# Optimization experiments

Measured on AMD Instinct MI355X. Metric: run time of the kernel, lower is better.

## Reference

```python
import jax, jax.numpy as jnp
import numpy as np

N_NODES = 50000
N_EDGES = 625000
HIDDEN = 128
NUM_GRAPHS = 128
EPS = 1e-5


def setup_inputs() -> dict:
    key = jax.random.key(0)
    ks = jax.random.split(key, 8)
    node = jax.random.normal(ks[0], (N_NODES, HIDDEN), dtype=jnp.float32)
    edge_index = jax.random.randint(ks[1], (2, N_EDGES), 0, N_NODES, dtype=jnp.int64)
    edge_attr = jax.random.uniform(ks[2], (N_EDGES,), dtype=jnp.float32)
    batch_ptr = jnp.sort(jax.random.randint(ks[3], (N_NODES,), 0, NUM_GRAPHS, dtype=jnp.int64))
    # GCNConv linear: weight [out,in], bias [out]
    W = jax.random.normal(ks[4], (HIDDEN, HIDDEN), dtype=jnp.float32) * (1.0 / np.sqrt(HIDDEN))
    b = jnp.zeros((HIDDEN,), dtype=jnp.float32)
    # GraphNorm params
    gn_weight = 1.0 + 0.02 * jax.random.normal(ks[5], (HIDDEN,), dtype=jnp.float32)
    gn_bias = 0.05 * jax.random.normal(ks[6], (HIDDEN,), dtype=jnp.float32)
    gn_mean_scale = 1.0 + 0.02 * jax.random.normal(ks[7], (HIDDEN,), dtype=jnp.float32)
    return {"node": node, "edge_index": edge_index, "edge_attr": edge_attr,
            "batch_ptr": batch_ptr, "W": W, "b": b,
            "gn_weight": gn_weight, "gn_bias": gn_bias, "gn_mean_scale": gn_mean_scale}


def _gcn_conv(x, src, dst, w, W, b):
    n = x.shape[0]
    # add self loops with weight 1
    loop = jnp.arange(n, dtype=src.dtype)
    src = jnp.concatenate([src, loop])
    dst = jnp.concatenate([dst, loop])
    w = jnp.concatenate([w, jnp.ones((n,), dtype=w.dtype)])
    # symmetric degree normalization (degrees at target nodes)
    deg = jax.ops.segment_sum(w, dst, num_segments=n)
    dinv = jnp.where(deg > 0, jax.lax.rsqrt(deg), 0.0)
    norm = dinv[src] * w * dinv[dst]  # [E+n]
    h = x @ W.T  # [n, d]
    msg = norm[:, None] * h[src]  # gather + scale
    out = jax.ops.segment_sum(msg, dst, num_segments=n)  # scatter-add
    return out + b


def _graph_norm(x, batch, weight, bias, mean_scale):
    cnt = jax.ops.segment_sum(jnp.ones((x.shape[0],), x.dtype), batch, num_segments=NUM_GRAPHS)
    cnt = jnp.maximum(cnt, 1.0)[:, None]
    mean = jax.ops.segment_sum(x, batch, num_segments=NUM_GRAPHS) / cnt
    centered = x - mean_scale * mean[batch]
    var = jax.ops.segment_sum(centered * centered, batch, num_segments=NUM_GRAPHS) / cnt
    inv_std = jax.lax.rsqrt(var + EPS)[batch]
    return weight * centered * inv_std + bias


def reference(node, edge_index, edge_attr, batch_ptr, W, b, gn_weight, gn_bias, gn_mean_scale):
    src, dst = edge_index[0], edge_index[1]
    h = _gcn_conv(node, src, dst, edge_attr, W, b)
    h = _graph_norm(h, batch_ptr, gn_weight, gn_bias, gn_mean_scale)
    return jax.nn.relu(h)
```

## Files before the change

### kernel.cpp

```cpp
#include <hip/hip_runtime.h>

#define N_NODES    50000
#define N_EDGES    625000
#define HIDDEN     128
#define NUM_GRAPHS 128
#define EPS_GN     1e-5f
#define FIXSCALE32 65536.0f
#define NGEMM_BLK  782
#define NHIST_BLK  306
#define NB_SCAN    196

typedef __bf16 bf16x8 __attribute__((ext_vector_type(8)));
typedef float  f32x4  __attribute__((ext_vector_type(4)));
typedef unsigned short u16x8 __attribute__((ext_vector_type(8)));
typedef unsigned long long u64;

__device__ inline unsigned short f2b(float f) {
    __bf16 b = (__bf16)f;
    return __builtin_bit_cast(unsigned short, b);
}
__device__ inline float b2f(unsigned short u) {
    unsigned int x = ((unsigned int)u) << 16;
    return __builtin_bit_cast(float, x);
}

#define HB_OFF     0
#define CNT_OFF    3200000
#define BSUM_OFF   3250000
#define DONE_OFF   3250256
#define DINV_OFF   3250260
#define WB_OFF     3300260
#define GSTART_OFF 3308452
#define ROWS_OFF   3308581
#define EPACK_OFF  3358582
#define SLOT_OFF   4608582
#define TMP_OFF    4608584

__global__ void prep(const float* __restrict__ W, unsigned short* __restrict__ wb,
                     uint4* __restrict__ z) {
    int i = blockIdx.x * 256 + threadIdx.x;
    if (i < 12565) z[i] = make_uint4(0u, 0u, 0u, 0u);
    if (i < HIDDEN * HIDDEN) wb[i] = f2b(W[i]);
}

__global__ __launch_bounds__(256) void gemm_hist(const float* __restrict__ x,
                                                 const unsigned short* __restrict__ wb,
                                                 unsigned short* __restrict__ hb,
                                                 const int* __restrict__ dst,
                                                 const float* __restrict__ w,
                                                 unsigned int* __restrict__ cnt32,
                                                 unsigned int* __restrict__ slot) {
    if (blockIdx.x >= NGEMM_BLK) {
        int base = (blockIdx.x - NGEMM_BLK) * 256 + threadIdx.x;
        if (base * 8 >= N_EDGES) return;
        int4   dA = ((const int4*)dst)[base * 2];
        int4   dB = ((const int4*)dst)[base * 2 + 1];
        float4 wA = ((const float4*)w)[base * 2];
        float4 wB = ((const float4*)w)[base * 2 + 1];
        uint4 sA, sB;
        unsigned int fx;
        fx = (unsigned int)(wA.x * FIXSCALE32 + 0.5f);
        sA.x = atomicAdd(&cnt32[dA.x], (1u << 24) | fx) >> 24;
        fx = (unsigned int)(wA.y * FIXSCALE32 + 0.5f);
        sA.y = atomicAdd(&cnt32[dA.y], (1u << 24) | fx) >> 24;
        fx = (unsigned int)(wA.z * FIXSCALE32 + 0.5f);
        sA.z = atomicAdd(&cnt32[dA.z], (1u << 24) | fx) >> 24;
        fx = (unsigned int)(wA.w * FIXSCALE32 + 0.5f);
        sA.w = atomicAdd(&cnt32[dA.w], (1u << 24) | fx) >> 24;
        fx = (unsigned int)(wB.x * FIXSCALE32 + 0.5f);
        sB.x = atomicAdd(&cnt32[dB.x], (1u << 24) | fx) >> 24;
        fx = (unsigned int)(wB.y * FIXSCALE32 + 0.5f);
        sB.y = atomicAdd(&cnt32[dB.y], (1u << 24) | fx) >> 24;
        fx = (unsigned int)(wB.z * FIXSCALE32 + 0.5f);
        sB.z = atomicAdd(&cnt32[dB.z], (1u << 24) | fx) >> 24;
        fx = (unsigned int)(wB.w * FIXSCALE32 + 0.5f);
        sB.w = atomicAdd(&cnt32[dB.w], (1u << 24) | fx) >> 24;
        ((uint4*)slot)[base * 2]     = sA;
        ((uint4*)slot)[base * 2 + 1] = sB;
        return;
    }
    const int wave = threadIdx.x >> 6;
    const int lane = threadIdx.x & 63;
    const int row0 = blockIdx.x * 64 + wave * 16;
    const int r  = lane & 15;
    const int ko = (lane >> 4) * 8;
    f32x4 acc[8];
#pragma unroll
    for (int t = 0; t < 8; ++t) { acc[t][0] = 0.f; acc[t][1] = 0.f; acc[t][2] = 0.f; acc[t][3] = 0.f; }
    int arow = row0 + r;
    if (arow >= N_NODES) arow = N_NODES - 1;
    const size_t abase = (size_t)arow * HIDDEN + ko;
#pragma unroll
    for (int kt = 0; kt < HIDDEN; kt += 32) {
        float4 a0 = *(const float4*)(x + abase + kt);
        float4 a1 = *(const float4*)(x + abase + kt + 4);
        bf16x8 a;
        a[0] = (__bf16)a0.x; a[1] = (__bf16)a0.y; a[2] = (__bf16)a0.z; a[3] = (__bf16)a0.w;
        a[4] = (__bf16)a1.x; a[5] = (__bf16)a1.y; a[6] = (__bf16)a1.z; a[7] = (__bf16)a1.w;
#pragma unroll
        for (int t = 0; t < 8; ++t) {
            bf16x8 b = *(const bf16x8*)(wb + (size_t)(t * 16 + r) * HIDDEN + kt + ko);
            acc[t] = __builtin_amdgcn_mfma_f32_16x16x32_bf16(a, b, acc[t], 0, 0, 0);
        }
    }
    const int orow = row0 + (lane >> 4) * 4;
#pragma unroll
    for (int t = 0; t < 8; ++t) {
#pragma unroll
        for (int j = 0; j < 4; ++j) {
            int rr = orow + j;
            if (rr < N_NODES) hb[(size_t)rr * HIDDEN + t * 16 + r] = f2b(acc[t][j]);
        }
    }
}

__global__ __launch_bounds__(256) void scan_fused(const unsigned int* __restrict__ cnt32,
                                                  unsigned int* __restrict__ bsum,
                                                  unsigned int* __restrict__ done,
                                                  float* __restrict__ dinv,
                                                  const int* __restrict__ batch,
                                                  int* __restrict__ gstart,
                                                  int* __restrict__ rowstart) {
    __shared__ int red[256];
    __shared__ int sb[256];
    const int t = threadIdx.x;
    const int b = blockIdx.x;
    const int i = b * 256 + t;
    int c = 0;
    if (i < N_NODES) {
        unsigned int v = cnt32[i];
        c = (int)(v >> 24);
        dinv[i] = rsqrtf(1.0f + (float)(v & 0xFFFFFFu) * (1.0f / FIXSCALE32));
        int b0 = batch[i];
        int prev = (i == 0) ? -1 : batch[i - 1];
        for (int g = prev + 1; g <= b0; ++g) gstart[g] = i;
        if (i == N_NODES - 1) {
            for (int g = b0 + 1; g <= NUM_GRAPHS; ++g) gstart[g] = N_NODES;
        }
    }
    red[t] = c;
    __syncthreads();
    for (int off = 128; off > 0; off >>= 1) {
        if (t < off) red[t] += red[t + off];
        __syncthreads();
    }
    if (t == 0) {
        atomicExch(&bsum[b], (unsigned int)red[0]);
        __threadfence();
        atomicAdd(done, 1u);
        while (atomicAdd(done, 0u) < (unsigned int)NB_SCAN) { }
    }
    __syncthreads();
    sb[t] = (t < NB_SCAN) ? (int)atomicAdd(&bsum[t], 0u) : 0;
    __syncthreads();
    for (int off = 1; off < 256; off <<= 1) {
        int v = (t >= off) ? sb[t - off] : 0;
        __syncthreads();
        sb[t] += v;
        __syncthreads();
    }
    int boff = (b == 0) ? 0 : sb[b - 1];
    __shared__ int s[256];
    s[t] = c;
    __syncthreads();
    for (int off = 1; off < 256; off <<= 1) {
        int v = (t >= off) ? s[t - off] : 0;
        __syncthreads();
        s[t] += v;
        __syncthreads();
    }
    if (i < N_NODES) rowstart[i] = boff + s[t] - c;
    if (i == N_NODES) rowstart[N_NODES] = N_EDGES;
}

__global__ void csr_fill(const int* __restrict__ src, const int* __restrict__ dst,
                         const float* __restrict__ w, const float* __restrict__ dinv,
                         const int* __restrict__ rowstart, const unsigned int* __restrict__ slot,
                         u64* __restrict__ epack) {
    int base = blockIdx.x * blockDim.x + threadIdx.x;
    if (base * 4 >= N_EDGES) return;
    int4   s4 = ((const int4*)src)[base];
    int4   d4 = ((const int4*)dst)[base];
    float4 w4 = ((const float4*)w)[base];
    uint4  r4 = ((const uint4*)slot)[base];
    float nm0 = dinv[s4.x] * w4.x * dinv[d4.x];
    float nm1 = dinv[s4.y] * w4.y * dinv[d4.y];
    float nm2 = dinv[s4.z] * w4.z * dinv[d4.z];
    float nm3 = dinv[s4.w] * w4.w * dinv[d4.w];
    epack[rowstart[d4.x] + (int)r4.x] = (u64)(unsigned int)s4.x | ((u64)__float_as_uint(nm0) << 32);
    epack[rowstart[d4.y] + (int)r4.y] = (u64)(unsigned int)s4.y | ((u64)__float_as_uint(nm1) << 32);
    epack[rowstart[d4.z] + (int)r4.z] = (u64)(unsigned int)s4.z | ((u64)__float_as_uint(nm2) << 32);
    epack[rowstart[d4.w] + (int)r4.w] = (u64)(unsigned int)s4.w | ((u64)__float_as_uint(nm3) << 32);
}

__global__ __launch_bounds__(256) void gather_fused(const unsigned short* __restrict__ hb,
                                                    const int* __restrict__ rowstart,
                                                    const u64* __restrict__ epack,
                                                    const float* __restrict__ dinv,
                                                    const float* __restrict__ b,
                                                    unsigned short* __restrict__ tmp) {
    const int t = threadIdx.x;
    const int n = blockIdx.x * 16 + (t >> 4);
    if (n >= N_NODES) return;
    const int c8 = (t & 15) * 8;
    const int s0 = rowstart[n];
    const int e0 = rowstart[n + 1];
    const float di = dinv[n];
    const float sl = di * di;
    float acc[8];
    {
        u16x8 hv = *(const u16x8*)(hb + (size_t)n * HIDDEN + c8);
#pragma unroll
        for (int j = 0; j < 8; ++j) acc[j] = sl * b2f(hv[j]);
    }
    int p = s0;
    for (; p + 4 <= e0; p += 4) {
        u64 e1 = epack[p];
        u64 e2 = epack[p + 1];
        u64 e3 = epack[p + 2];
        u64 e4 = epack[p + 3];
        int   x1 = (int)(unsigned int)e1;
        int   x2 = (int)(unsigned int)e2;
        int   x3 = (int)(unsigned int)e3;
        int   x4 = (int)(unsigned int)e4;
        float n1 = __uint_as_float((unsigned int)(e1 >> 32));
        float n2 = __uint_as_float((unsigned int)(e2 >> 32));
        float n3 = __uint_as_float((unsigned int)(e3 >> 32));
        float n4 = __uint_as_float((unsigned int)(e4 >> 32));
        u16x8 v1 = *(const u16x8*)(hb + (size_t)x1 * HIDDEN + c8);
        u16x8 v2 = *(const u16x8*)(hb + (size_t)x2 * HIDDEN + c8);
        u16x8 v3 = *(const u16x8*)(hb + (size_t)x3 * HIDDEN + c8);
        u16x8 v4 = *(const u16x8*)(hb + (size_t)x4 * HIDDEN + c8);
#pragma unroll
        for (int j = 0; j < 8; ++j) acc[j] = fmaf(n1, b2f(v1[j]), acc[j]);
#pragma unroll
        for (int j = 0; j < 8; ++j) acc[j] = fmaf(n2, b2f(v2[j]), acc[j]);
#pragma unroll
        for (int j = 0; j < 8; ++j) acc[j] = fmaf(n3, b2f(v3[j]), acc[j]);
#pragma unroll
        for (int j = 0; j < 8; ++j) acc[j] = fmaf(n4, b2f(v4[j]), acc[j]);
    }
    for (; p < e0; ++p) {
        u64 e1 = epack[p];
        int   x1 = (int)(unsigned int)e1;
        float n1 = __uint_as_float((unsigned int)(e1 >> 32));
        u16x8 v1 = *(const u16x8*)(hb + (size_t)x1 * HIDDEN + c8);
#pragma unroll
        for (int j = 0; j < 8; ++j) acc[j] = fmaf(n1, b2f(v1[j]), acc[j]);
    }
    float4 b0 = *(const float4*)(b + c8);
    float4 b1 = *(const float4*)(b + c8 + 4);
    u16x8 o;
    o[0] = f2b(acc[0] + b0.x); o[1] = f2b(acc[1] + b0.y);
    o[2] = f2b(acc[2] + b0.z); o[3] = f2b(acc[3] + b0.w);
    o[4] = f2b(acc[4] + b1.x); o[5] = f2b(acc[5] + b1.y);
    o[6] = f2b(acc[6] + b1.z); o[7] = f2b(acc[7] + b1.w);
    *(u16x8*)(tmp + (size_t)n * HIDDEN + c8) = o;
}

__global__ __launch_bounds__(256) void stats_apply(const unsigned short* __restrict__ tmp,
                                                   const int* __restrict__ gstart,
                                                   const float* __restrict__ ms,
                                                   const float* __restrict__ gw,
                                                   const float* __restrict__ gb,
                                                   float* __restrict__ out) {
    const int g = blockIdx.x >> 2;
    const int q = blockIdx.x & 3;
    const int l = threadIdx.x & 31;
    const int c = q * 32 + l;
    const int r = threadIdx.x >> 5;
    const int s = gstart[g];
    const int e = gstart[g + 1];
    float sum = 0.f, sq = 0.f;
    for (int n = s + r; n < e; n += 8) {
        float v = b2f(tmp[(size_t)n * HIDDEN + c]);
        sum += v;
        sq = fmaf(v, v, sq);
    }
    __shared__ float ssum[8][32], ssq[8][32];
    __shared__ float sA[32], sS[32];
    ssum[r][l] = sum;
    ssq[r][l]  = sq;
    __syncthreads();
    if (r == 0) {
#pragma unroll
        for (int i = 1; i < 8; ++i) { sum += ssum[i][l]; sq += ssq[i][l]; }
        float cnt  = (float)max(e - s, 1);
        float mean = sum / cnt;
        float m2   = sq / cnt;
        float msv  = ms[c];
        float var  = fmaxf(m2 - mean * mean * msv * (2.f - msv), 0.f);
        float a    = gw[c] * rsqrtf(var + EPS_GN);
        sA[l] = a;
        sS[l] = gb[c] - a * msv * mean;
    }
    __syncthreads();
    float a  = sA[l];
    float sh = sS[l];
    for (int n = s + r; n < e; n += 8) {
        float v = b2f(tmp[(size_t)n * HIDDEN + c]);
        out[(size_t)n * HIDDEN + c] = fmaxf(fmaf(a, v, sh), 0.f);
    }
}

extern "C" void kernel_launch(void* const* d_in, const int* in_sizes, int n_in,
                              void* d_out, int out_size, void* d_ws, size_t ws_size,
                              hipStream_t stream) {
    const float* node  = (const float*)d_in[0];
    const int*   ei    = (const int*)d_in[1];
    const float* eattr = (const float*)d_in[2];
    const int*   batch = (const int*)d_in[3];
    const float* W     = (const float*)d_in[4];
    const float* b     = (const float*)d_in[5];
    const float* gnw   = (const float*)d_in[6];
    const float* gnb   = (const float*)d_in[7];
    const float* gnms  = (const float*)d_in[8];
    float* out = (float*)d_out;
    float* ws  = (float*)d_ws;

    const int* src = ei;
    const int* dst = ei + N_EDGES;

    unsigned short* hb = (unsigned short*)(ws + HB_OFF);
    unsigned int* cnt32 = (unsigned int*)(ws + CNT_OFF);
    unsigned int* bsum  = (unsigned int*)(ws + BSUM_OFF);
    unsigned int* done  = (unsigned int*)(ws + DONE_OFF);
    float* dinv    = ws + DINV_OFF;
    unsigned short* wb = (unsigned short*)(ws + WB_OFF);
    int*   gstart  = (int*)(ws + GSTART_OFF);
    int*   rowstart= (int*)(ws + ROWS_OFF);
    u64*   epack   = (u64*)(ws + EPACK_OFF);
    unsigned int* slot = (unsigned int*)(ws + SLOT_OFF);
    unsigned short* tmp = (unsigned short*)(ws + TMP_OFF);

    prep<<<98, 256, 0, stream>>>(W, wb, (uint4*)cnt32);
    gemm_hist<<<NGEMM_BLK + NHIST_BLK, 256, 0, stream>>>(node, wb, hb, dst, eattr, cnt32, slot);
    scan_fused<<<NB_SCAN, 256, 0, stream>>>(cnt32, bsum, done, dinv, batch, gstart, rowstart);
    csr_fill<<<(N_EDGES / 4 + 255) / 256, 256, 0, stream>>>(src, dst, eattr, dinv, rowstart, slot, epack);
    gather_fused<<<(N_NODES + 15) / 16, 256, 0, stream>>>(hb, rowstart, epack, dinv, b, tmp);
    stats_apply<<<NUM_GRAPHS * 4, 256, 0, stream>>>(tmp, gstart, gnms, gnw, gnb, out);

    (void)in_sizes; (void)n_in; (void)out_size; (void)ws_size;
}
```

Baseline: 127.2 us.

## Split node range into two halves and software-pipeline stages across fused launches

Splits the destination nodes into two halves and interleaves the stages: histogram, scan, CSR fill, gather and stats for half A run in the same launch as the previous stage for half B. The aim is to fill the GPU during the small, latency-bound stages (scan, stats) and hide the gaps between launches. The source-side dinv is moved from CSR fill into the gather, because with split scans dinv for the second half may not be ready during CSR fill of half A. Each pass now scans all edges twice with a predicate, and the stats split assumes graphs do not straddle the boundary in a harmful way. The scan also waits on a spin barrier, so it needs all of its blocks to be resident at the same time as the other blocks in the launch.

```diff
diff --git a/kernel.cpp b/kernel.cpp
--- a/kernel.cpp
+++ b/kernel.cpp
@@ -6,9 +6,12 @@
 #define NUM_GRAPHS 128
 #define EPS_GN     1e-5f
 #define FIXSCALE32 65536.0f
+#define NSPLIT     25000
 #define NGEMM_BLK  782
 #define NHIST_BLK  306
-#define NB_SCAN    196
+#define NCSR_BLK   611
+#define NB_HALF    98
+#define NGATH_BLK  1563
 
 typedef __bf16 bf16x8 __attribute__((ext_vector_type(8)));
 typedef float  f32x4  __attribute__((ext_vector_type(4)));
@@ -26,108 +29,63 @@
 
 #define HB_OFF     0
 #define CNT_OFF    3200000
-#define BSUM_OFF   3250000
-#define DONE_OFF   3250256
-#define DINV_OFF   3250260
-#define WB_OFF     3300260
-#define GSTART_OFF 3308452
-#define ROWS_OFF   3308581
-#define EPACK_OFF  3358582
-#define SLOT_OFF   4608582
-#define TMP_OFF    4608584
+#define DONE_OFF   3250000
+#define BSUMA_OFF  3250008
+#define BSUMB_OFF  3250136
+#define DINV_OFF   3250264
+#define WB_OFF     3300264
+#define GSTART_OFF 3308456
+#define ROWS_OFF   3308585
+#define EPACK_OFF  3358586
+#define SLOT_OFF   4608588
+#define TMP_OFF    5233588
 
 __global__ void prep(const float* __restrict__ W, unsigned short* __restrict__ wb,
                      uint4* __restrict__ z) {
     int i = blockIdx.x * 256 + threadIdx.x;
-    if (i < 12565) z[i] = make_uint4(0u, 0u, 0u, 0u);
+    if (i < 12502) z[i] = make_uint4(0u, 0u, 0u, 0u);
     if (i < HIDDEN * HIDDEN) wb[i] = f2b(W[i]);
 }
 
-__global__ __launch_bounds__(256) void gemm_hist(const float* __restrict__ x,
-                                                 const unsigned short* __restrict__ wb,
-                                                 unsigned short* __restrict__ hb,
-                                                 const int* __restrict__ dst,
-                                                 const float* __restrict__ w,
-                                                 unsigned int* __restrict__ cnt32,
-                                                 unsigned int* __restrict__ slot) {
-    if (blockIdx.x >= NGEMM_BLK) {
-        int base = (blockIdx.x - NGEMM_BLK) * 256 + threadIdx.x;
-        if (base * 8 >= N_EDGES) return;
-        int4   dA = ((const int4*)dst)[base * 2];
-        int4   dB = ((const int4*)dst)[base * 2 + 1];
-        float4 wA = ((const float4*)w)[base * 2];
-        float4 wB = ((const float4*)w)[base * 2 + 1];
-        uint4 sA, sB;
-        unsigned int fx;
-        fx = (unsigned int)(wA.x * FIXSCALE32 + 0.5f);
-        sA.x = atomicAdd(&cnt32[dA.x], (1u << 24) | fx) >> 24;
-        fx = (unsigned int)(wA.y * FIXSCALE32 + 0.5f);
-        sA.y = atomicAdd(&cnt32[dA.y], (1u << 24) | fx) >> 24;
-        fx = (unsigned int)(wA.z * FIXSCALE32 + 0.5f);
-        sA.z = atomicAdd(&cnt32[dA.z], (1u << 24) | fx) >> 24;
-        fx = (unsigned int)(wA.w * FIXSCALE32 + 0.5f);
-        sA.w = atomicAdd(&cnt32[dA.w], (1u << 24) | fx) >> 24;
-        fx = (unsigned int)(wB.x * FIXSCALE32 + 0.5f);
-        sB.x = atomicAdd(&cnt32[dB.x], (1u << 24) | fx) >> 24;
-        fx = (unsigned int)(wB.y * FIXSCALE32 + 0.5f);
-        sB.y = atomicAdd(&cnt32[dB.y], (1u << 24) | fx) >> 24;
-        fx = (unsigned int)(wB.z * FIXSCALE32 + 0.5f);
-        sB.z = atomicAdd(&cnt32[dB.z], (1u << 24) | fx) >> 24;
-        fx = (unsigned int)(wB.w * FIXSCALE32 + 0.5f);
-        sB.w = atomicAdd(&cnt32[dB.w], (1u << 24) | fx) >> 24;
-        ((uint4*)slot)[base * 2]     = sA;
-        ((uint4*)slot)[base * 2 + 1] = sB;
-        return;
-    }
-    const int wave = threadIdx.x >> 6;
-    const int lane = threadIdx.x & 63;
-    const int row0 = blockIdx.x * 64 + wave * 16;
-    const int r  = lane & 15;
-    const int ko = (lane >> 4) * 8;
-    f32x4 acc[8];
-#pragma unroll
-    for (int t = 0; t < 8; ++t) { acc[t][0] = 0.f; acc[t][1] = 0.f; acc[t][2] = 0.f; acc[t][3] = 0.f; }
-    int arow = row0 + r;
-    if (arow >= N_NODES) arow = N_NODES - 1;
-    const size_t abase = (size_t)arow * HIDDEN + ko;
-#pragma unroll
-    for (int kt = 0; kt < HIDDEN; kt += 32) {
-        float4 a0 = *(const float4*)(x + abase + kt);
-        float4 a1 = *(const float4*)(x + abase + kt + 4);
-        bf16x8 a;
-        a[0] = (__bf16)a0.x; a[1] = (__bf16)a0.y; a[2] = (__bf16)a0.z; a[3] = (__bf16)a0.w;
-        a[4] = (__bf16)a1.x; a[5] = (__bf16)a1.y; a[6] = (__bf16)a1.z; a[7] = (__bf16)a1.w;
-#pragma unroll
-        for (int t = 0; t < 8; ++t) {
-            bf16x8 b = *(const bf16x8*)(wb + (size_t)(t * 16 + r) * HIDDEN + kt + ko);
-            acc[t] = __builtin_amdgcn_mfma_f32_16x16x32_bf16(a, b, acc[t], 0, 0, 0);
-        }
-    }
-    const int orow = row0 + (lane >> 4) * 4;
-#pragma unroll
-    for (int t = 0; t < 8; ++t) {
-#pragma unroll
-        for (int j = 0; j < 4; ++j) {
-            int rr = orow + j;
-            if (rr < N_NODES) hb[(size_t)rr * HIDDEN + t * 16 + r] = f2b(acc[t][j]);
-        }
-    }
-}
-
-__global__ __launch_bounds__(256) void scan_fused(const unsigned int* __restrict__ cnt32,
-                                                  unsigned int* __restrict__ bsum,
-                                                  unsigned int* __restrict__ done,
-                                                  float* __restrict__ dinv,
-                                                  const int* __restrict__ batch,
-                                                  int* __restrict__ gstart,
-                                                  int* __restrict__ rowstart) {
+__device__ inline void hist_pass(int blk, const int* __restrict__ dst,
+                                 const float* __restrict__ w,
+                                 unsigned int* __restrict__ cnt32,
+                                 unsigned int* __restrict__ slot, bool isA) {
+    int base = blk * 256 + threadIdx.x;
+    if (base * 8 >= N_EDGES) return;
+    int4   d0 = ((const int4*)dst)[base * 2];
+    int4   d1 = ((const int4*)dst)[base * 2 + 1];
+    float4 w0 = ((const float4*)w)[base * 2];
+    float4 w1 = ((const float4*)w)[base * 2 + 1];
+    int e0 = base * 8;
+#define HPROC(EI, DV, WV)                                                        \
+    if (((DV) < NSPLIT) == isA) {                                                \
+        unsigned int fx = (unsigned int)((WV) * FIXSCALE32 + 0.5f);              \
+        slot[EI] = atomicAdd(&cnt32[DV], (1u << 24) | fx) >> 24;                 \
+    }
+    HPROC(e0 + 0, d0.x, w0.x) HPROC(e0 + 1, d0.y, w0.y)
+    HPROC(e0 + 2, d0.z, w0.z) HPROC(e0 + 3, d0.w, w0.w)
+    HPROC(e0 + 4, d1.x, w1.x) HPROC(e0 + 5, d1.y, w1.y)
+    HPROC(e0 + 6, d1.z, w1.z) HPROC(e0 + 7, d1.w, w1.w)
+#undef HPROC
+}
+
+__device__ inline void scan_half(int sbid, int nbase,
+                                 const unsigned int* __restrict__ cnt32,
+                                 unsigned int* __restrict__ bsum,
+                                 unsigned int* __restrict__ done,
+                                 float* __restrict__ dinv,
+                                 const int* __restrict__ batch,
+                                 int* __restrict__ gstart,
+                                 int* __restrict__ rowstart) {
     __shared__ int red[256];
-    __shared__ int sb[256];
+    __shared__ int sb[128];
+    __shared__ int s[256];
     const int t = threadIdx.x;
-    const int b = blockIdx.x;
-    const int i = b * 256 + t;
+    const int i = nbase + sbid * 256 + t;
+    const int iend = nbase + NSPLIT;
     int c = 0;
-    if (i < N_NODES) {
+    if (i < iend) {
         unsigned int v = cnt32[i];
         c = (int)(v >> 24);
         dinv[i] = rsqrtf(1.0f + (float)(v & 0xFFFFFFu) * (1.0f / FIXSCALE32));
@@ -145,22 +103,23 @@
         __syncthreads();
     }
     if (t == 0) {
-        atomicExch(&bsum[b], (unsigned int)red[0]);
+        atomicExch(&bsum[sbid], (unsigned int)red[0]);
         __threadfence();
         atomicAdd(done, 1u);
-        while (atomicAdd(done, 0u) < (unsigned int)NB_SCAN) { }
-    }
-    __syncthreads();
-    sb[t] = (t < NB_SCAN) ? (int)atomicAdd(&bsum[t], 0u) : 0;
-    __syncthreads();
-    for (int off = 1; off < 256; off <<= 1) {
-        int v = (t >= off) ? sb[t - off] : 0;
-        __syncthreads();
-        sb[t] += v;
-        __syncthreads();
-    }
-    int boff = (b == 0) ? 0 : sb[b - 1];
-    __shared__ int s[256];
+        while (atomicAdd(done, 0u) < (unsigned int)NB_HALF) {
+            __builtin_amdgcn_s_sleep(2);
+        }
+    }
+    __syncthreads();
+    if (t < NB_HALF) sb[t] = (int)atomicAdd(&bsum[t], 0u);
+    __syncthreads();
+    if (t == 0) {
+        int acc = 0;
+        for (int k = 0; k < NB_HALF; ++k) { acc += sb[k]; sb[k] = acc; }
+    }
+    __syncthreads();
+    int ebase = (nbase == 0) ? 0 : rowstart[nbase];
+    int boff = ebase + ((sbid == 0) ? 0 : sb[sbid - 1]);
     s[t] = c;
     __syncthreads();
     for (int off = 1; off < 256; off <<= 1) {
@@ -169,39 +128,49 @@
         s[t] += v;
         __syncthreads();
     }
-    if (i < N_NODES) rowstart[i] = boff + s[t] - c;
-    if (i == N_NODES) rowstart[N_NODES] = N_EDGES;
-}
-
-__global__ void csr_fill(const int* __restrict__ src, const int* __restrict__ dst,
-                         const float* __restrict__ w, const float* __restrict__ dinv,
-                         const int* __restrict__ rowstart, const unsigned int* __restrict__ slot,
-                         u64* __restrict__ epack) {
-    int base = blockIdx.x * blockDim.x + threadIdx.x;
+    if (i < iend) rowstart[i] = boff + s[t] - c;
+    if (sbid == NB_HALF - 1 && t == 0) {
+        if (nbase == 0) rowstart[NSPLIT] = sb[NB_HALF - 1];
+        else            rowstart[N_NODES] = N_EDGES;
+    }
+}
+
+__device__ inline void csr_pass(int blk, const int* __restrict__ src,
+                                const int* __restrict__ dst,
+                                const float* __restrict__ w,
+                                const float* __restrict__ dinv,
+                                const int* __restrict__ rowstart,
+                                const unsigned int* __restrict__ slot,
+                                u64* __restrict__ epack, bool isA) {
+    int base = blk * 256 + threadIdx.x;
     if (base * 4 >= N_EDGES) return;
     int4   s4 = ((const int4*)src)[base];
     int4   d4 = ((const int4*)dst)[base];
     float4 w4 = ((const float4*)w)[base];
     uint4  r4 = ((const uint4*)slot)[base];
-    float nm0 = dinv[s4.x] * w4.x * dinv[d4.x];
-    float nm1 = dinv[s4.y] * w4.y * dinv[d4.y];
-    float nm2 = dinv[s4.z] * w4.z * dinv[d4.z];
-    float nm3 = dinv[s4.w] * w4.w * dinv[d4.w];
-    epack[rowstart[d4.x] + (int)r4.x] = (u64)(unsigned int)s4.x | ((u64)__float_as_uint(nm0) << 32);
-    epack[rowstart[d4.y] + (int)r4.y] = (u64)(unsigned int)s4.y | ((u64)__float_as_uint(nm1) << 32);
-    epack[rowstart[d4.z] + (int)r4.z] = (u64)(unsigned int)s4.z | ((u64)__float_as_uint(nm2) << 32);
-    epack[rowstart[d4.w] + (int)r4.w] = (u64)(unsigned int)s4.w | ((u64)__float_as_uint(nm3) << 32);
-}
-
-__global__ __launch_bounds__(256) void gather_fused(const unsigned short* __restrict__ hb,
-                                                    const int* __restrict__ rowstart,
-                                                    const u64* __restrict__ epack,
-                                                    const float* __restrict__ dinv,
-                                                    const float* __restrict__ b,
-                                                    unsigned short* __restrict__ tmp) {
+#define CPROC(SV, DV, WV, RV)                                                     \
+    if (((DV) < NSPLIT) == isA) {                                                 \
+        float pn = (WV) * dinv[DV];                                               \
+        epack[rowstart[DV] + (int)(RV)] =                                         \
+            (u64)(unsigned int)(SV) | ((u64)__float_as_uint(pn) << 32);           \
+    }
+    CPROC(s4.x, d4.x, w4.x, r4.x)
+    CPROC(s4.y, d4.y, w4.y, r4.y)
+    CPROC(s4.z, d4.z, w4.z, r4.z)
+    CPROC(s4.w, d4.w, w4.w, r4.w)
+#undef CPROC
+}
+
+__device__ inline void gather_body(int gblk, int nbase,
+                                   const unsigned short* __restrict__ hb,
+                                   const int* __restrict__ rowstart,
+                                   const u64* __restrict__ epack,
+                                   const float* __restrict__ dinv,
+                                   const float* __restrict__ b,
+                                   unsigned short* __restrict__ tmp) {
     const int t = threadIdx.x;
-    const int n = blockIdx.x * 16 + (t >> 4);
-    if (n >= N_NODES) return;
+    const int n = nbase + gblk * 16 + (t >> 4);
+    if (n >= nbase + NSPLIT || n >= N_NODES) return;
     const int c8 = (t & 15) * 8;
     const int s0 = rowstart[n];
     const int e0 = rowstart[n + 1];
@@ -219,14 +188,14 @@
         u64 e2 = epack[p + 1];
         u64 e3 = epack[p + 2];
         u64 e4 = epack[p + 3];
-        int   x1 = (int)(unsigned int)e1;
-        int   x2 = (int)(unsigned int)e2;
-        int   x3 = (int)(unsigned int)e3;
-        int   x4 = (int)(unsigned int)e4;
-        float n1 = __uint_as_float((unsigned int)(e1 >> 32));
-        float n2 = __uint_as_float((unsigned int)(e2 >> 32));
-        float n3 = __uint_as_float((unsigned int)(e3 >> 32));
-        float n4 = __uint_as_float((unsigned int)(e4 >> 32));
+        int x1 = (int)(unsigned int)e1;
+        int x2 = (int)(unsigned int)e2;
+        int x3 = (int)(unsigned int)e3;
+        int x4 = (int)(unsigned int)e4;
+        float n1 = __uint_as_float((unsigned int)(e1 >> 32)) * dinv[x1];
+        float n2 = __uint_as_float((unsigned int)(e2 >> 32)) * dinv[x2];
+        float n3 = __uint_as_float((unsigned int)(e3 >> 32)) * dinv[x3];
+        float n4 = __uint_as_float((unsigned int)(e4 >> 32)) * dinv[x4];
         u16x8 v1 = *(const u16x8*)(hb + (size_t)x1 * HIDDEN + c8);
         u16x8 v2 = *(const u16x8*)(hb + (size_t)x2 * HIDDEN + c8);
         u16x8 v3 = *(const u16x8*)(hb + (size_t)x3 * HIDDEN + c8);
@@ -242,8 +211,8 @@
     }
     for (; p < e0; ++p) {
         u64 e1 = epack[p];
-        int   x1 = (int)(unsigned int)e1;
-        float n1 = __uint_as_float((unsigned int)(e1 >> 32));
+        int x1 = (int)(unsigned int)e1;
+        float n1 = __uint_as_float((unsigned int)(e1 >> 32)) * dinv[x1];
         u16x8 v1 = *(const u16x8*)(hb + (size_t)x1 * HIDDEN + c8);
 #pragma unroll
         for (int j = 0; j < 8; ++j) acc[j] = fmaf(n1, b2f(v1[j]), acc[j]);
@@ -258,19 +227,21 @@
     *(u16x8*)(tmp + (size_t)n * HIDDEN + c8) = o;
 }
 
-__global__ __launch_bounds__(256) void stats_apply(const unsigned short* __restrict__ tmp,
-                                                   const int* __restrict__ gstart,
-                                                   const float* __restrict__ ms,
-                                                   const float* __restrict__ gw,
-                                                   const float* __restrict__ gb,
-                                                   float* __restrict__ out) {
-    const int g = blockIdx.x >> 2;
-    const int q = blockIdx.x & 3;
+__device__ inline void stats_body(int sblk,
+                                  const unsigned short* __restrict__ tmp,
+                                  const int* __restrict__ gstart,
+                                  const float* __restrict__ ms,
+                                  const float* __restrict__ gw,
+                                  const float* __restrict__ gb,
+                                  float* __restrict__ out, bool phaseA) {
+    const int g = sblk >> 2;
+    const int q = sblk & 3;
     const int l = threadIdx.x & 31;
     const int c = q * 32 + l;
     const int r = threadIdx.x >> 5;
     const int s = gstart[g];
     const int e = gstart[g + 1];
+    if ((e <= NSPLIT) != phaseA) return;
     float sum = 0.f, sq = 0.f;
     for (int n = s + r; n < e; n += 8) {
         float v = b2f(tmp[(size_t)n * HIDDEN + c]);
@@ -301,6 +272,136 @@
         float v = b2f(tmp[(size_t)n * HIDDEN + c]);
         out[(size_t)n * HIDDEN + c] = fmaxf(fmaf(a, v, sh), 0.f);
     }
+}
+
+
+__global__ __launch_bounds__(256) void d1_gemm_histA(const float* __restrict__ x,
+                                                     const unsigned short* __restrict__ wb,
+                                                     unsigned short* __restrict__ hb,
+                                                     const int* __restrict__ dst,
+                                                     const float* __restrict__ w,
+                                                     unsigned int* __restrict__ cnt32,
+                                                     unsigned int* __restrict__ slot) {
+    if (blockIdx.x >= NGEMM_BLK) {
+        hist_pass(blockIdx.x - NGEMM_BLK, dst, w, cnt32, slot, true);
+        return;
+    }
+    const int wave = threadIdx.x >> 6;
+    const int lane = threadIdx.x & 63;
+    const int row0 = blockIdx.x * 64 + wave * 16;
+    const int r  = lane & 15;
+    const int ko = (lane >> 4) * 8;
+    f32x4 acc[8];
+#pragma unroll
+    for (int t = 0; t < 8; ++t) { acc[t][0] = 0.f; acc[t][1] = 0.f; acc[t][2] = 0.f; acc[t][3] = 0.f; }
+    int arow = row0 + r;
+    if (arow >= N_NODES) arow = N_NODES - 1;
+    const size_t abase = (size_t)arow * HIDDEN + ko;
+#pragma unroll
+    for (int kt = 0; kt < HIDDEN; kt += 32) {
+        float4 a0 = *(const float4*)(x + abase + kt);
+        float4 a1 = *(const float4*)(x + abase + kt + 4);
+        bf16x8 a;
+        a[0] = (__bf16)a0.x; a[1] = (__bf16)a0.y; a[2] = (__bf16)a0.z; a[3] = (__bf16)a0.w;
+        a[4] = (__bf16)a1.x; a[5] = (__bf16)a1.y; a[6] = (__bf16)a1.z; a[7] = (__bf16)a1.w;
+#pragma unroll
+        for (int t = 0; t < 8; ++t) {
+            bf16x8 b = *(const bf16x8*)(wb + (size_t)(t * 16 + r) * HIDDEN + kt + ko);
+            acc[t] = __builtin_amdgcn_mfma_f32_16x16x32_bf16(a, b, acc[t], 0, 0, 0);
+        }
+    }
+    const int orow = row0 + (lane >> 4) * 4;
+#pragma unroll
+    for (int t = 0; t < 8; ++t) {
+#pragma unroll
+        for (int j = 0; j < 4; ++j) {
+            int rr = orow + j;
+            if (rr < N_NODES) hb[(size_t)rr * HIDDEN + t * 16 + r] = f2b(acc[t][j]);
+        }
+    }
+}
+
+__global__ __launch_bounds__(256) void d2_histB_scanA(const int* __restrict__ dst,
+                                                      const float* __restrict__ w,
+                                                      unsigned int* __restrict__ cnt32,
+                                                      unsigned int* __restrict__ slot,
+                                                      unsigned int* __restrict__ bsumA,
+                                                      unsigned int* __restrict__ done,
+                                                      float* __restrict__ dinv,
+                                                      const int* __restrict__ batch,
+                                                      int* __restrict__ gstart,
+                                                      int* __restrict__ rowstart) {
+    if (blockIdx.x < NHIST_BLK) {
+        hist_pass(blockIdx.x, dst, w, cnt32, slot, false);
+        return;
+    }
+    scan_half(blockIdx.x - NHIST_BLK, 0, cnt32, bsumA, done, dinv, batch, gstart, rowstart);
+}
+
+__global__ __launch_bounds__(256) void d3_csrA_scanB(const int* __restrict__ src,
+                                                     const int* __restrict__ dst,
+                                                     const float* __restrict__ w,
+                                                     const float* __restrict__ dinv,
+                                                     const int* __restrict__ rowstart,
+                                                     const unsigned int* __restrict__ slot,
+                                                     u64* __restrict__ epack,
+                                                     const unsigned int* __restrict__ cnt32,
+                                                     unsigned int* __restrict__ bsumB,
+                                                     unsigned int* __restrict__ done,
+                                                     const int* __restrict__ batch,
+                                                     int* __restrict__ gstart,
+                                                     float* __restrict__ dinv_w,
+                                                     int* __restrict__ rowstart_w) {
+    if (blockIdx.x < NCSR_BLK) {
+        csr_pass(blockIdx.x, src, dst, w, dinv, rowstart, slot, epack, true);
+        return;
+    }
+    scan_half(blockIdx.x - NCSR_BLK, NSPLIT, cnt32, bsumB, done, dinv_w, batch, gstart, rowstart_w);
+}
+
+__global__ __launch_bounds__(256) void d4_gatherA_csrB(const unsigned short* __restrict__ hb,
+                                                       const int* __restrict__ rowstart,
+                                                       const u64* __restrict__ epack,
+                                                       const float* __restrict__ dinv,
+                                                       const float* __restrict__ b,
+                                                       unsigned short* __restrict__ tmp,
+                                                       const int* __restrict__ src,
+                                                       const int* __restrict__ dst,
+                                                       const float* __restrict__ w,
+                                                       const unsigned int* __restrict__ slot,
+                                                       u64* __restrict__ epack_w) {
+    if (blockIdx.x < NGATH_BLK) {
+        gather_body(blockIdx.x, 0, hb, rowstart, epack, dinv, b, tmp);
+        return;
+    }
+    csr_pass(blockIdx.x - NGATH_BLK, src, dst, w, dinv, rowstart, slot, epack_w, false);
+}
+
+__global__ __launch_bounds__(256) void d5_gatherB_statsA(const unsigned short* __restrict__ hb,
+                                                         const int* __restrict__ rowstart,
+                                                         const u64* __restrict__ epack,
+                                                         const float* __restrict__ dinv,
+                                                         const float* __restrict__ b,
+                                                         unsigned short* __restrict__ tmp,
+                                                         const int* __restrict__ gstart,
+                                                         const float* __restrict__ ms,
+                                                         const float* __restrict__ gw,
+                                                         const float* __restrict__ gb,
+                                                         float* __restrict__ out) {
+    if (blockIdx.x < NGATH_BLK) {
+        gather_body(blockIdx.x, NSPLIT, hb, rowstart, epack, dinv, b, tmp);
+        return;
+    }
+    stats_body(blockIdx.x - NGATH_BLK, tmp, gstart, ms, gw, gb, out, true);
+}
+
+__global__ __launch_bounds__(256) void d6_statsB(const unsigned short* __restrict__ tmp,
+                                                 const int* __restrict__ gstart,
+                                                 const float* __restrict__ ms,
+                                                 const float* __restrict__ gw,
+                                                 const float* __restrict__ gb,
+                                                 float* __restrict__ out) {
+    stats_body(blockIdx.x, tmp, gstart, ms, gw, gb, out, false);
 }
 
 extern "C" void kernel_launch(void* const* d_in, const int* in_sizes, int n_in,
@@ -321,24 +422,31 @@
     const int* src = ei;
     const int* dst = ei + N_EDGES;
 
-    unsigned short* hb = (unsigned short*)(ws + HB_OFF);
-    unsigned int* cnt32 = (unsigned int*)(ws + CNT_OFF);
-    unsigned int* bsum  = (unsigned int*)(ws + BSUM_OFF);
-    unsigned int* done  = (unsigned int*)(ws + DONE_OFF);
-    float* dinv    = ws + DINV_OFF;
-    unsigned short* wb = (unsigned short*)(ws + WB_OFF);
-    int*   gstart  = (int*)(ws + GSTART_OFF);
-    int*   rowstart= (int*)(ws + ROWS_OFF);
-    u64*   epack   = (u64*)(ws + EPACK_OFF);
-    unsigned int* slot = (unsigned int*)(ws + SLOT_OFF);
-    unsigned short* tmp = (unsigned short*)(ws + TMP_OFF);
+    unsigned short* hb   = (unsigned short*)(ws + HB_OFF);
+    unsigned int*  cnt32 = (unsigned int*)(ws + CNT_OFF);
+    unsigned int*  done  = (unsigned int*)(ws + DONE_OFF);
+    unsigned int*  bsumA = (unsigned int*)(ws + BSUMA_OFF);
+    unsigned int*  bsumB = (unsigned int*)(ws + BSUMB_OFF);
+    float* dinv          = ws + DINV_OFF;
+    unsigned short* wb   = (unsigned short*)(ws + WB_OFF);
+    int*   gstart        = (int*)(ws + GSTART_OFF);
+    int*   rowstart      = (int*)(ws + ROWS_OFF);
+    u64*   epack         = (u64*)(ws + EPACK_OFF);
+    unsigned int* slot   = (unsigned int*)(ws + SLOT_OFF);
+    unsigned short* tmp  = (unsigned short*)(ws + TMP_OFF);
 
     prep<<<98, 256, 0, stream>>>(W, wb, (uint4*)cnt32);
-    gemm_hist<<<NGEMM_BLK + NHIST_BLK, 256, 0, stream>>>(node, wb, hb, dst, eattr, cnt32, slot);
-    scan_fused<<<NB_SCAN, 256, 0, stream>>>(cnt32, bsum, done, dinv, batch, gstart, rowstart);
-    csr_fill<<<(N_EDGES / 4 + 255) / 256, 256, 0, stream>>>(src, dst, eattr, dinv, rowstart, slot, epack);
-    gather_fused<<<(N_NODES + 15) / 16, 256, 0, stream>>>(hb, rowstart, epack, dinv, b, tmp);
-    stats_apply<<<NUM_GRAPHS * 4, 256, 0, stream>>>(tmp, gstart, gnms, gnw, gnb, out);
+    d1_gemm_histA<<<NGEMM_BLK + NHIST_BLK, 256, 0, stream>>>(node, wb, hb, dst, eattr, cnt32, slot);
+    d2_histB_scanA<<<NHIST_BLK + NB_HALF, 256, 0, stream>>>(dst, eattr, cnt32, slot, bsumA, done,
+                                                            dinv, batch, gstart, rowstart);
+    d3_csrA_scanB<<<NCSR_BLK + NB_HALF, 256, 0, stream>>>(src, dst, eattr, dinv, rowstart, slot, epack,
+                                                          cnt32, bsumB, done + 1, batch, gstart,
+                                                          dinv, rowstart);
+    d4_gatherA_csrB<<<NGATH_BLK + NCSR_BLK, 256, 0, stream>>>(hb, rowstart, epack, dinv, b, tmp,
+                                                              src, dst, eattr, slot, epack);
+    d5_gatherB_statsA<<<NGATH_BLK + 512, 256, 0, stream>>>(hb, rowstart, epack, dinv, b, tmp,
+                                                           gstart, gnms, gnw, gnb, out);
+    d6_statsB<<<512, 256, 0, stream>>>(tmp, gstart, gnms, gnw, gnb, out);
 
     (void)in_sizes; (void)n_in; (void)out_size; (void)ws_size;
 }
```

Result: slower. 163.1 us (+28.3%).
